# Optimization experiments

Hardware: AMD Instinct MI355X
Metric: run time of the kernel (lower is better)

## Reference

```python
import jax, jax.numpy as jnp
import numpy as np

NUM_HEADS = 4
SPATIAL_DS = 2
EPS = 1e-5


def setup_inputs() -> dict:
    key = jax.random.key(0)
    ks = jax.random.split(key, 6)
    B, C, H, W = 8, 256, 64, 64
    hd = C // NUM_HEADS
    return {
        "x": jax.random.normal(ks[0], (B, C, H, W), jnp.float32),
        "gn_w": jnp.ones((C,), jnp.float32),
        "gn_b": jnp.zeros((C,), jnp.float32),
        "wq": jax.random.normal(ks[1], (C, C), jnp.float32) * (C ** -0.5),
        "wk": jax.random.normal(ks[2], (hd, C), jnp.float32) * (C ** -0.5),
        "wv": jax.random.normal(ks[3], (hd, C), jnp.float32) * (C ** -0.5),
        "wo": jax.random.normal(ks[4], (C, C), jnp.float32) * (C ** -0.5),
        "gamma": jnp.full((C,), 1e-4, jnp.float32),
    }


def reference(x, gn_w, gn_b, wq, wk, wv, wo, gamma):
    B, C, H, W = x.shape
    hd = C // NUM_HEADS
    scale = hd ** -0.5
    ds = SPATIAL_DS

    # GroupNorm with 1 group: normalize over (C,H,W) per sample, per-channel affine
    mu = jnp.mean(x, axis=(1, 2, 3), keepdims=True)
    var = jnp.var(x, axis=(1, 2, 3), keepdims=True)
    xn = (x - mu) * jax.lax.rsqrt(var + EPS)
    xn = xn * gn_w[None, :, None, None] + gn_b[None, :, None, None]

    # Q projection (1x1 conv == channel matmul): (B, heads, N, hd)
    q = jnp.einsum('oc,bchw->bohw', wq, xn).reshape(B, NUM_HEADS, hd, H * W)
    q = jnp.swapaxes(q, 2, 3)  # (B, h, N, hd)

    # AvgPool2d(ds, ds) on normalized input for K/V
    Hd, Wd = H // ds, W // ds
    x_ds = xn.reshape(B, C, Hd, ds, Wd, ds).mean(axis=(3, 5))

    k = jnp.einsum('oc,bchw->bohw', wk, x_ds).reshape(B, hd, Hd * Wd)
    k = jnp.swapaxes(k, 1, 2)  # (B, M, hd) single shared head
    v = jnp.einsum('oc,bchw->bohw', wv, x_ds).reshape(B, hd, Hd * Wd)
    v = jnp.swapaxes(v, 1, 2)  # (B, M, hd)

    # Multi-query attention: queries per-head, shared K/V
    attn = jnp.einsum('bhnd,bmd->bhnm', q, k) * scale
    attn = jax.nn.softmax(attn, axis=-1)
    out = jnp.einsum('bhnm,bmd->bhnd', attn, v)  # (B, h, N, hd)

    out = jnp.swapaxes(out, 2, 3).reshape(B, C, H, W)
    out = jnp.einsum('oc,bchw->bohw', wo, out)

    return x + out * gamma[None, :, None, None]
```

## Files before the change

kernel.cpp:

```cpp
#include <hip/hip_runtime.h>


#define CNT_INV (1.0f/1048576.0f)
#define EPSV 1e-5f
#define QSCALE 0.18033688f

#define WS_STATS 0
#define WS_XNT   64
#define WS_XDS   4194368
#define WS_K     5242944
#define WS_V     5505088
#define WS_WQB   5767232
#define WS_WKV   5800000
#define WS_WOB   5816384

typedef __attribute__((ext_vector_type(8))) short bf8_t;
typedef __attribute__((ext_vector_type(4))) float f4_t;

static __device__ __forceinline__ unsigned fbits(float f) {
  union { float f; unsigned u; } v; v.f = f; return v.u;
}
static __device__ __forceinline__ unsigned short f2bf(float f) {
  unsigned u = fbits(f);
  return (unsigned short)((u + 0x7fffu + ((u >> 16) & 1u)) >> 16);
}
static __device__ __forceinline__ unsigned pk_rnd(float a, float b) {
  return __builtin_amdgcn_perm(fbits(b) + 0x8000u, fbits(a) + 0x8000u, 0x07060302u);
}
static __device__ __forceinline__ unsigned pk_tr(float a, float b) {
  return __builtin_amdgcn_perm(fbits(b), fbits(a), 0x07060302u);
}
static __device__ __forceinline__ float bf2f(unsigned short h) {
  union { unsigned u; float f; } v; v.u = ((unsigned)h) << 16; return v.f;
}
static __device__ __forceinline__ float fexp2(float x) {
  float r; asm("v_exp_f32 %0, %1" : "=v"(r) : "v"(x)); return r;
}

__global__ __launch_bounds__(256) void k_prep_stats(const float* __restrict__ x,
                                                    const float* __restrict__ wq,
                                                    const float* __restrict__ wk,
                                                    const float* __restrict__ wv,
                                                    const float* __restrict__ wo,
                                                    float* __restrict__ stats,
                                                    unsigned short* __restrict__ wqb,
                                                    unsigned short* __restrict__ wkvb,
                                                    unsigned short* __restrict__ wob) {
  const int blk = blockIdx.x;
  const int t = threadIdx.x;
  if (blk < 512) {
    const int b = blk >> 6;
    const int chunk = blk & 63;
    const float4* xb = (const float4*)(x + (size_t)b * 1048576 + (size_t)chunk * 16384);
    float s = 0.f, s2 = 0.f;
#pragma unroll
    for (int it = 0; it < 16; ++it) {
      float4 v = xb[it * 256 + t];
      s  += v.x + v.y + v.z + v.w;
      s2 += v.x * v.x + v.y * v.y + v.z * v.z + v.w * v.w;
    }
#pragma unroll
    for (int o = 32; o > 0; o >>= 1) {
      s  += __shfl_down(s, o);
      s2 += __shfl_down(s2, o);
    }
    __shared__ float red[8];
    const int wid = t >> 6;
    if ((t & 63) == 0) { red[wid] = s; red[4 + wid] = s2; }
    __syncthreads();
    if (t == 0) {
      atomicAdd(&stats[b * 2 + 0], red[0] + red[1] + red[2] + red[3]);
      atomicAdd(&stats[b * 2 + 1], red[4] + red[5] + red[6] + red[7]);
    }
  } else {
    const int idx = (blk - 512) * 256 + t;
    if (idx < 65536) wqb[idx] = f2bf(wq[idx]);
    else if (idx < 81920) wkvb[idx - 65536] = f2bf(wk[idx - 65536]);
    else if (idx < 98304) wkvb[idx - 65536] = f2bf(wv[idx - 81920]);
    else if (idx < 163840) wob[idx - 98304] = f2bf(wo[idx - 98304]);
  }
}

__global__ __launch_bounds__(256) void k_xnt(const float* __restrict__ x,
                                             const float* __restrict__ gnw,
                                             const float* __restrict__ gnb,
                                             const float* __restrict__ stats,
                                             unsigned short* __restrict__ xnT,
                                             unsigned short* __restrict__ xdsT) {
  __shared__ unsigned short T[128][72];
  const int t = threadIdx.x;
  const int b = blockIdx.z, c0 = blockIdx.y * 64, hp = blockIdx.x;
  const int n0 = hp * 128;
  const float mu = stats[b * 2 + 0] * CNT_INV;
  const float rstd = rsqrtf(stats[b * 2 + 1] * CNT_INV - mu * mu + EPSV);
  const int n4 = (t & 31) * 4, cl = t >> 5;
  const int wswz = t & 7;
#pragma unroll
  for (int p = 0; p < 8; ++p) {
    const int c = c0 + p * 8 + cl;
    const float gw = gnw[c] * rstd;
    const float gb = gnb[c] - mu * rstd * gnw[c];
    const int pc = (p ^ wswz) * 8 + cl;
    float4 v = *(const float4*)&x[(size_t)(b * 256 + c) * 4096 + n0 + n4];
    T[n4 + 0][pc] = f2bf(v.x * gw + gb);
    T[n4 + 1][pc] = f2bf(v.y * gw + gb);
    T[n4 + 2][pc] = f2bf(v.z * gw + gb);
    T[n4 + 3][pc] = f2bf(v.w * gw + gb);
  }
  __syncthreads();
  {
    const int r = t >> 1, cb4 = (t & 1) * 4;
    const int rswz = (t >> 3) & 7;
    unsigned short* dst = xnT + ((size_t)b * 4096 + n0 + r) * 256 + c0 + cb4 * 8;
#pragma unroll
    for (int u = 0; u < 4; ++u)
      *(uint4*)(dst + u * 8) = *(const uint4*)&T[r][((cb4 + u) ^ rswz) * 8];
  }
  {
    const int wd = t >> 3, c8 = t & 7;
    const int pswz = (wd >> 1) & 7;
    const int pc = (c8 ^ pswz) * 8;
    uint4 u0 = *(const uint4*)&T[2 * wd][pc];
    uint4 u1 = *(const uint4*)&T[2 * wd + 1][pc];
    uint4 u2 = *(const uint4*)&T[64 + 2 * wd][pc];
    uint4 u3 = *(const uint4*)&T[64 + 2 * wd + 1][pc];
    const unsigned* p0 = (const unsigned*)&u0; const unsigned* p1 = (const unsigned*)&u1;
    const unsigned* p2 = (const unsigned*)&u2; const unsigned* p3 = (const unsigned*)&u3;
    unsigned outp[4];
#pragma unroll
    for (int i = 0; i < 4; ++i) {
      float lo = (bf2f((unsigned short)p0[i]) + bf2f((unsigned short)p1[i]) +
                  bf2f((unsigned short)p2[i]) + bf2f((unsigned short)p3[i])) * 0.25f;
      float hi = (bf2f((unsigned short)(p0[i] >> 16)) + bf2f((unsigned short)(p1[i] >> 16)) +
                  bf2f((unsigned short)(p2[i] >> 16)) + bf2f((unsigned short)(p3[i] >> 16))) * 0.25f;
      outp[i] = pk_rnd(lo, hi);
    }
    *(uint4*)(xdsT + ((size_t)b * 1024 + hp * 32 + wd) * 256 + c0 + c8 * 8) = *(uint4*)outp;
  }
}

__global__ __launch_bounds__(256) void k_gemm_kv(const unsigned short* __restrict__ wkvb,
                                                 const unsigned short* __restrict__ xdsT,
                                                 unsigned short* __restrict__ kbf,
                                                 unsigned short* __restrict__ vtbf) {
  __shared__ __align__(16) unsigned short kv[2][64][72];
  const int t = threadIdx.x;
  const int w = t >> 6, l = t & 63, lane16 = l & 15, quad = l >> 4;
  const int m0 = blockIdx.x * 64, b = blockIdx.y;
  const unsigned short* Abase = wkvb + (size_t)(w * 32 + lane16) * 256 + quad * 8;
  const unsigned short* Bbase = xdsT + ((size_t)b * 1024 + m0 + lane16) * 256 + quad * 8;
  f4_t acc[2][4];
#pragma unroll
  for (int i = 0; i < 2; ++i)
#pragma unroll
    for (int j = 0; j < 4; ++j) acc[i][j] = (f4_t){0.f, 0.f, 0.f, 0.f};
  bf8_t Ac[2], Bc[4];
#pragma unroll
  for (int og = 0; og < 2; ++og) Ac[og] = *(const bf8_t*)(Abase + (size_t)og * 16 * 256);
#pragma unroll
  for (int mg = 0; mg < 4; ++mg) Bc[mg] = *(const bf8_t*)(Bbase + (size_t)mg * 16 * 256);
  for (int kc = 0; kc < 256; kc += 32) {
    const int kn = (kc + 32) & 255;
    bf8_t An[2], Bn[4];
#pragma unroll
    for (int og = 0; og < 2; ++og) An[og] = *(const bf8_t*)(Abase + (size_t)og * 16 * 256 + kn);
#pragma unroll
    for (int mg = 0; mg < 4; ++mg) Bn[mg] = *(const bf8_t*)(Bbase + (size_t)mg * 16 * 256 + kn);
#pragma unroll
    for (int og = 0; og < 2; ++og)
#pragma unroll
      for (int mg = 0; mg < 4; ++mg)
        acc[og][mg] = __builtin_amdgcn_mfma_f32_16x16x32_bf16(Ac[og], Bc[mg], acc[og][mg], 0, 0, 0);
#pragma unroll
    for (int og = 0; og < 2; ++og) Ac[og] = An[og];
#pragma unroll
    for (int mg = 0; mg < 4; ++mg) Bc[mg] = Bn[mg];
  }
  if (w < 2) {
#pragma unroll
    for (int og = 0; og < 2; ++og)
#pragma unroll
      for (int mg = 0; mg < 4; ++mg) {
        uint2 p;
        p.x = pk_rnd(acc[og][mg][0], acc[og][mg][1]);
        p.y = pk_rnd(acc[og][mg][2], acc[og][mg][3]);
        *(uint2*)&kv[0][mg * 16 + lane16][w * 32 + og * 16 + quad * 4] = p;
      }
  } else {
#pragma unroll
    for (int og = 0; og < 2; ++og)
#pragma unroll
      for (int mg = 0; mg < 4; ++mg) {
        const int d0 = (w - 2) * 32 + og * 16 + quad * 4;
#pragma unroll
        for (int r = 0; r < 4; ++r)
          kv[1][d0 + r][mg * 16 + lane16] = f2bf(acc[og][mg][r]);
      }
  }
  __syncthreads();
  {
    const int row = t >> 2, q2 = t & 3;
    const int e = row & 7;
    uint4 k0 = *(const uint4*)&kv[0][row][q2 * 16];
    uint4 k1 = *(const uint4*)&kv[0][row][q2 * 16 + 8];
    unsigned short* kd = kbf + (size_t)b * 65536 + (size_t)(m0 + row) * 64;
    *(uint4*)(kd + ((q2 * 2) ^ e) * 8)     = k0;
    *(uint4*)(kd + ((q2 * 2 + 1) ^ e) * 8) = k1;
    uint4 v0 = *(const uint4*)&kv[1][row][q2 * 16];
    uint4 v1 = *(const uint4*)&kv[1][row][q2 * 16 + 8];
    unsigned short* vd = vtbf + (size_t)b * 65536 + (size_t)(blockIdx.x * 2 + (q2 >> 1)) * 2048 +
                         (size_t)row * 32 + (q2 & 1) * 16;
    *(uint4*)vd = v0; *(uint4*)(vd + 8) = v1;
  }
}

__global__ __launch_bounds__(256) void k_fused(const unsigned short* __restrict__ wqb,
                                               const unsigned short* __restrict__ xnT,
                                               const unsigned short* __restrict__ kbf,
                                               const unsigned short* __restrict__ vtbf,
                                               const unsigned short* __restrict__ wob,
                                               const float* __restrict__ x,
                                               const float* __restrict__ gamma,
                                               float* __restrict__ outp) {
  __shared__ __align__(16) unsigned short smem[20480];
  __shared__ __align__(16) unsigned short kst[2][2048];
  __shared__ __align__(16) unsigned short vst[2][2048];
  const int t = threadIdx.x;
  const int w = t >> 6, l = t & 63, lane16 = l & 15, quad = l >> 4;
  const int n0 = blockIdx.x * 64, b = blockIdx.y;
  const int h = w;
  unsigned short* qst = smem + w * 4608;
  unsigned short (*plds)[64][40] = (unsigned short (*)[64][40])(smem + w * 5120);
  unsigned short (*aos)[264] = (unsigned short (*)[264])smem;

  const int sw = w & 1;
  const unsigned short* sbase = (w < 2) ? (kbf + (size_t)b * 65536) : (vtbf + (size_t)b * 65536);
  unsigned short* sdst0 = ((w < 2) ? &kst[0][0] : &vst[0][0]) + sw * 1024 + l * 8;
  unsigned short* sdst1 = ((w < 2) ? &kst[1][0] : &vst[1][0]) + sw * 1024 + l * 8;

#define STAGE_ISSUE(WIN, R0, R1)                                              \
  { const unsigned short* sp = sbase + (size_t)(WIN) * 2048 + sw * 1024 + l * 8; \
    R0 = *(const uint4*)sp; R1 = *(const uint4*)(sp + 512); }
#define STAGE_WRITE(DP, R0, R1)                                               \
  { *(uint4*)(DP) = R0; *(uint4*)((DP) + 512) = R1; }

#define READ_K(BUF, KREG)                                                     \
  {                                                                           \
    _Pragma("unroll")                                                         \
    for (int s = 0; s < 2; ++s) {                                             \
      _Pragma("unroll")                                                       \
      for (int dc = 0; dc < 2; ++dc)                                          \
        KREG[s][dc] = *(const bf8_t*)&kst[BUF][(s * 16 + lane16) * 64 +       \
                                              (((dc * 4 + quad) ^ (lane16 & 7)) * 8)]; \
    }                                                                         \
  }
#define READ_V(BUF, VREG)                                                     \
  {                                                                           \
    _Pragma("unroll")                                                         \
    for (int dg = 0; dg < 4; ++dg)                                            \
      VREG[dg] = *(const bf8_t*)&vst[BUF][(dg * 16 + lane16) * 32 + quad * 8]; \
  }

  const unsigned short* kb = kbf;

  {
    const unsigned short* Abase = wqb + (size_t)(h * 64 + lane16) * 256 + quad * 8;
    const unsigned short* Bbase = xnT + ((size_t)b * 4096 + n0 + lane16) * 256 + quad * 8;
    f4_t qacc[4][4];
#pragma unroll
    for (int i = 0; i < 4; ++i)
#pragma unroll
      for (int j = 0; j < 4; ++j) qacc[i][j] = (f4_t){0.f, 0.f, 0.f, 0.f};
    for (int kc = 0; kc < 256; kc += 32) {
      bf8_t A[4], Bf[4];
#pragma unroll
      for (int og = 0; og < 4; ++og) A[og] = *(const bf8_t*)(Abase + (size_t)og * 16 * 256 + kc);
#pragma unroll
      for (int ng = 0; ng < 4; ++ng) Bf[ng] = *(const bf8_t*)(Bbase + (size_t)ng * 16 * 256 + kc);
#pragma unroll
      for (int og = 0; og < 4; ++og)
#pragma unroll
        for (int ng = 0; ng < 4; ++ng)
          qacc[og][ng] = __builtin_amdgcn_mfma_f32_16x16x32_bf16(A[og], Bf[ng], qacc[og][ng], 0, 0, 0);
    }
#pragma unroll
    for (int og = 0; og < 4; ++og)
#pragma unroll
      for (int ng = 0; ng < 4; ++ng) {
        uint2 p;
        p.x = pk_rnd(qacc[og][ng][0] * QSCALE, qacc[og][ng][1] * QSCALE);
        p.y = pk_rnd(qacc[og][ng][2] * QSCALE, qacc[og][ng][3] * QSCALE);
        *(uint2*)&qst[(ng * 16 + lane16) * 72 + og * 16 + quad * 4] = p;
      }
  }
  bf8_t Qf[4][2];
#pragma unroll
  for (int qg = 0; qg < 4; ++qg)
#pragma unroll
    for (int dc = 0; dc < 2; ++dc)
      Qf[qg][dc] = *(const bf8_t*)&qst[(qg * 16 + lane16) * 72 + dc * 32 + quad * 8];
  __syncthreads();

  f4_t O[4][4];
#pragma unroll
  for (int dg = 0; dg < 4; ++dg)
#pragma unroll
    for (int qg = 0; qg < 4; ++qg) O[dg][qg] = (f4_t){0.f, 0.f, 0.f, 0.f};
  f4_t O4[4];
#pragma unroll
  for (int qg = 0; qg < 4; ++qg) O4[qg] = (f4_t){0.f, 0.f, 0.f, 0.f};
  const short onebf = (lane16 == 0) ? (short)0x3F80 : (short)0;
  const bf8_t Aone = {onebf, onebf, onebf, onebf, onebf, onebf, onebf, onebf};

#define SSTEP(KREG, BUF)                                                      \
  {                                                                           \
    _Pragma("unroll")                                                         \
    for (int qg = 0; qg < 4; ++qg) {                                          \
      _Pragma("unroll")                                                       \
      for (int s = 0; s < 2; ++s) {                                           \
        f4_t S = (f4_t){0.f, 0.f, 0.f, 0.f};                                  \
        S = __builtin_amdgcn_mfma_f32_16x16x32_bf16(KREG[s][0], Qf[qg][0], S, 0, 0, 0); \
        S = __builtin_amdgcn_mfma_f32_16x16x32_bf16(KREG[s][1], Qf[qg][1], S, 0, 0, 0); \
        float e0 = fexp2(S[0]);                                               \
        float e1 = fexp2(S[1]);                                               \
        float e2 = fexp2(S[2]);                                               \
        float e3 = fexp2(S[3]);                                               \
        uint2 p; p.x = pk_tr(e0, e1); p.y = pk_tr(e2, e3);                    \
        *(uint2*)&plds[BUF][qg * 16 + lane16][s * 16 + quad * 4] = p;         \
      }                                                                       \
    }                                                                         \
  }

  {
    uint4 a0, a1, b0, b1;
    STAGE_ISSUE(0, a0, a1);
    STAGE_ISSUE(1, b0, b1);
    STAGE_WRITE(sdst0, a0, a1);
    STAGE_WRITE(sdst1, b0, b1);
  }
  __syncthreads();

  bf8_t Kc[2][2], Vc[4];
  READ_K(0, Kc);
  SSTEP(Kc, 0);
  READ_V(0, Vc);
  __syncthreads();

  for (int it = 1; it < 32; ++it) {
    const int cur = it & 1, pb = cur ^ 1;
    uint4 g0, g1;
    if (it < 31) STAGE_ISSUE(it + 1, g0, g1);
    bf8_t Pf[4];
#pragma unroll
    for (int qg = 0; qg < 4; ++qg)
      Pf[qg] = *(const bf8_t*)&plds[pb][qg * 16 + lane16][quad * 8];
    READ_K(cur, Kc);
    bf8_t Vn[4];
    READ_V(cur, Vn);
    __builtin_amdgcn_s_setprio(1);
#pragma unroll
    for (int dg = 0; dg < 4; ++dg)
#pragma unroll
      for (int qg = 0; qg < 4; ++qg)
        O[dg][qg] = __builtin_amdgcn_mfma_f32_16x16x32_bf16(Vc[dg], Pf[qg], O[dg][qg], 0, 0, 0);
#pragma unroll
    for (int qg = 0; qg < 4; ++qg)
      O4[qg] = __builtin_amdgcn_mfma_f32_16x16x32_bf16(Aone, Pf[qg], O4[qg], 0, 0, 0);
    __builtin_amdgcn_s_setprio(0);
    SSTEP(Kc, cur);
#pragma unroll
    for (int dg = 0; dg < 4; ++dg) Vc[dg] = Vn[dg];
    if (it < 31) STAGE_WRITE((cur ? sdst0 : sdst1), g0, g1);
    __syncthreads();
  }
  {
    bf8_t Pf[4];
#pragma unroll
    for (int qg = 0; qg < 4; ++qg)
      Pf[qg] = *(const bf8_t*)&plds[1][qg * 16 + lane16][quad * 8];
    __builtin_amdgcn_s_setprio(1);
#pragma unroll
    for (int dg = 0; dg < 4; ++dg)
#pragma unroll
      for (int qg = 0; qg < 4; ++qg)
        O[dg][qg] = __builtin_amdgcn_mfma_f32_16x16x32_bf16(Vc[dg], Pf[qg], O[dg][qg], 0, 0, 0);
#pragma unroll
    for (int qg = 0; qg < 4; ++qg)
      O4[qg] = __builtin_amdgcn_mfma_f32_16x16x32_bf16(Aone, Pf[qg], O4[qg], 0, 0, 0);
    __builtin_amdgcn_s_setprio(0);
  }
#undef SSTEP
#undef STAGE_ISSUE
#undef STAGE_WRITE
#undef READ_K
#undef READ_V
  (void)kb;

  float rden[4];
#pragma unroll
  for (int qg = 0; qg < 4; ++qg) {
    float d = __shfl(O4[qg][0], lane16);
    rden[qg] = 1.f / d;
  }

  __syncthreads();
#pragma unroll
  for (int dg = 0; dg < 4; ++dg)
#pragma unroll
    for (int qg = 0; qg < 4; ++qg) {
      const int c0 = h * 64 + dg * 16 + quad * 4;
      uint2 p;
      p.x = pk_rnd(O[dg][qg][0] * rden[qg], O[dg][qg][1] * rden[qg]);
      p.y = pk_rnd(O[dg][qg][2] * rden[qg], O[dg][qg][3] * rden[qg]);
      *(uint2*)&aos[qg * 16 + lane16][c0] = p;
    }
  __syncthreads();

  {
    const unsigned short* Wbase = wob + (size_t)(w * 64 + lane16) * 256 + quad * 8;
    f4_t acc[4][4];
#pragma unroll
    for (int i = 0; i < 4; ++i)
#pragma unroll
      for (int j = 0; j < 4; ++j) acc[i][j] = (f4_t){0.f, 0.f, 0.f, 0.f};
    for (int kc = 0; kc < 256; kc += 32) {
      bf8_t A[4], Bf[4];
#pragma unroll
      for (int og = 0; og < 4; ++og) A[og] = *(const bf8_t*)(Wbase + (size_t)og * 16 * 256 + kc);
#pragma unroll
      for (int ng = 0; ng < 4; ++ng) Bf[ng] = *(const bf8_t*)&aos[ng * 16 + lane16][kc + quad * 8];
#pragma unroll
      for (int og = 0; og < 4; ++og)
#pragma unroll
        for (int ng = 0; ng < 4; ++ng)
          acc[og][ng] = __builtin_amdgcn_mfma_f32_16x16x32_bf16(A[og], Bf[ng], acc[og][ng], 0, 0, 0);
    }
#pragma unroll
    for (int og = 0; og < 4; ++og) {
      float4 g4 = *(const float4*)&gamma[w * 64 + og * 16 + quad * 4];
      const float g[4] = {g4.x, g4.y, g4.z, g4.w};
#pragma unroll
      for (int ng = 0; ng < 4; ++ng) {
        const int n = n0 + ng * 16 + lane16;
#pragma unroll
        for (int r = 0; r < 4; ++r) {
          const int o = w * 64 + og * 16 + quad * 4 + r;
          const size_t ix = ((size_t)(b * 256 + o)) * 4096 + n;
          outp[ix] = x[ix] + g[r] * acc[og][ng][r];
        }
      }
    }
  }
}

extern "C" void kernel_launch(void* const* d_in, const int* in_sizes, int n_in,
                              void* d_out, int out_size, void* d_ws, size_t ws_size,
                              hipStream_t stream) {
  const float* x     = (const float*)d_in[0];
  const float* gnw   = (const float*)d_in[1];
  const float* gnb   = (const float*)d_in[2];
  const float* wq    = (const float*)d_in[3];
  const float* wk    = (const float*)d_in[4];
  const float* wv    = (const float*)d_in[5];
  const float* wo    = (const float*)d_in[6];
  const float* gamma = (const float*)d_in[7];
  float* out = (float*)d_out;
  float* ws  = (float*)d_ws;
  unsigned short* xnT  = (unsigned short*)(ws + WS_XNT);
  unsigned short* xdsT = (unsigned short*)(ws + WS_XDS);
  unsigned short* kbf  = (unsigned short*)(ws + WS_K);
  unsigned short* vtbf = (unsigned short*)(ws + WS_V);
  unsigned short* wqb  = (unsigned short*)(ws + WS_WQB);
  unsigned short* wkvb = (unsigned short*)(ws + WS_WKV);
  unsigned short* wob  = (unsigned short*)(ws + WS_WOB);

  hipMemsetAsync(ws, 0, 256, stream);
  k_prep_stats<<<1152, 256, 0, stream>>>(x, wq, wk, wv, wo, ws + WS_STATS, wqb, wkvb, wob);
  k_xnt<<<dim3(32, 4, 8), 256, 0, stream>>>(x, gnw, gnb, ws + WS_STATS, xnT, xdsT);
  k_gemm_kv<<<dim3(16, 8), 256, 0, stream>>>(wkvb, xdsT, kbf, vtbf);
  k_fused<<<dim3(64, 8), 256, 0, stream>>>(wqb, xnT, kbf, vtbf, wob, x, gamma, out);
}
```

Before: 194.1 us.

## Fold groupnorm affine and avgpool into consumer GEMMs, merge transpose into prep kernel

The raw x is now transposed to bf16 in the stats/prep kernel, which removes the separate normalize-and-transpose kernel and the pooled buffer. The GroupNorm affine is applied on the fly to the B operands in the Q GEMM inside the fused kernel. The 2x2 average pool plus affine is computed while loading operands in the KV GEMM, which now uses smaller tiles across more blocks. This saves a launch and a global round trip, at the cost of extra ALU work in the GEMM inner loops, more uncoalesced 4-way loads for the pooling, and bf16 rounding applied before normalization rather than after.

```diff
diff --git a/kernel.cpp b/kernel.cpp
--- a/kernel.cpp
+++ b/kernel.cpp
@@ -7,7 +7,6 @@
 
 #define WS_STATS 0
 #define WS_XNT   64
-#define WS_XDS   4194368
 #define WS_K     5242944
 #define WS_V     5505088
 #define WS_WQB   5767232
@@ -37,15 +36,47 @@
   float r; asm("v_exp_f32 %0, %1" : "=v"(r) : "v"(x)); return r;
 }
 
-__global__ __launch_bounds__(256) void k_prep_stats(const float* __restrict__ x,
-                                                    const float* __restrict__ wq,
-                                                    const float* __restrict__ wk,
-                                                    const float* __restrict__ wv,
-                                                    const float* __restrict__ wo,
-                                                    float* __restrict__ stats,
-                                                    unsigned short* __restrict__ wqb,
-                                                    unsigned short* __restrict__ wkvb,
-                                                    unsigned short* __restrict__ wob) {
+static __device__ __forceinline__ bf8_t affine8(bf8_t r, const float* a8, const float* b8) {
+  union { bf8_t v; unsigned short u[8]; unsigned w[4]; } in, out;
+  in.v = r;
+#pragma unroll
+  for (int i = 0; i < 4; ++i) {
+    float lo = fmaf(bf2f(in.u[2 * i]),     a8[2 * i],     b8[2 * i]);
+    float hi = fmaf(bf2f(in.u[2 * i + 1]), a8[2 * i + 1], b8[2 * i + 1]);
+    out.w[i] = pk_rnd(lo, hi);
+  }
+  return out.v;
+}
+
+static __device__ __forceinline__ bf8_t pool_affine(bf8_t s00, bf8_t s01, bf8_t s10, bf8_t s11,
+                                                    const float* a4, const float* b8) {
+  union { bf8_t v; unsigned short u[8]; unsigned w[4]; } x00, x01, x10, x11, out;
+  x00.v = s00; x01.v = s01; x10.v = s10; x11.v = s11;
+#pragma unroll
+  for (int i = 0; i < 4; ++i) {
+    float lo = (bf2f(x00.u[2 * i]) + bf2f(x01.u[2 * i])) +
+               (bf2f(x10.u[2 * i]) + bf2f(x11.u[2 * i]));
+    float hi = (bf2f(x00.u[2 * i + 1]) + bf2f(x01.u[2 * i + 1])) +
+               (bf2f(x10.u[2 * i + 1]) + bf2f(x11.u[2 * i + 1]));
+    lo = fmaf(lo, a4[2 * i],     b8[2 * i]);
+    hi = fmaf(hi, a4[2 * i + 1], b8[2 * i + 1]);
+    out.w[i] = pk_rnd(lo, hi);
+  }
+  return out.v;
+}
+
+__global__ __launch_bounds__(256) void k_prep(const float* __restrict__ x,
+                                              const float* __restrict__ wq,
+                                              const float* __restrict__ wk,
+                                              const float* __restrict__ wv,
+                                              const float* __restrict__ wo,
+                                              float* __restrict__ stats,
+                                              unsigned short* __restrict__ wqb,
+                                              unsigned short* __restrict__ wkvb,
+                                              unsigned short* __restrict__ wob,
+                                              unsigned short* __restrict__ xtb) {
+  __shared__ unsigned short T[128][72];
+  __shared__ float red[8];
   const int blk = blockIdx.x;
   const int t = threadIdx.x;
   if (blk < 512) {
@@ -64,7 +95,6 @@
       s  += __shfl_down(s, o);
       s2 += __shfl_down(s2, o);
     }
-    __shared__ float red[8];
     const int wid = t >> 6;
     if ((t & 63) == 0) { red[wid] = s; red[4 + wid] = s2; }
     __syncthreads();
@@ -72,150 +102,144 @@
       atomicAdd(&stats[b * 2 + 0], red[0] + red[1] + red[2] + red[3]);
       atomicAdd(&stats[b * 2 + 1], red[4] + red[5] + red[6] + red[7]);
     }
-  } else {
+  } else if (blk < 1152) {
     const int idx = (blk - 512) * 256 + t;
     if (idx < 65536) wqb[idx] = f2bf(wq[idx]);
     else if (idx < 81920) wkvb[idx - 65536] = f2bf(wk[idx - 65536]);
     else if (idx < 98304) wkvb[idx - 65536] = f2bf(wv[idx - 81920]);
     else if (idx < 163840) wob[idx - 98304] = f2bf(wo[idx - 98304]);
-  }
-}
-
-__global__ __launch_bounds__(256) void k_xnt(const float* __restrict__ x,
-                                             const float* __restrict__ gnw,
-                                             const float* __restrict__ gnb,
-                                             const float* __restrict__ stats,
-                                             unsigned short* __restrict__ xnT,
-                                             unsigned short* __restrict__ xdsT) {
-  __shared__ unsigned short T[128][72];
+  } else {
+    const int idx = blk - 1152;
+    const int hp = idx & 31, cq = (idx >> 5) & 3, b = idx >> 7;
+    const int c0 = cq * 64, n0 = hp * 128;
+    const int n4 = (t & 31) * 4, cl = t >> 5;
+    const int wswz = t & 7;
+#pragma unroll
+    for (int p = 0; p < 8; ++p) {
+      const int c = c0 + p * 8 + cl;
+      const int pc = (p ^ wswz) * 8 + cl;
+      float4 v = *(const float4*)&x[(size_t)(b * 256 + c) * 4096 + n0 + n4];
+      T[n4 + 0][pc] = f2bf(v.x);
+      T[n4 + 1][pc] = f2bf(v.y);
+      T[n4 + 2][pc] = f2bf(v.z);
+      T[n4 + 3][pc] = f2bf(v.w);
+    }
+    __syncthreads();
+    {
+      const int r = t >> 1, cb4 = (t & 1) * 4;
+      const int rswz = (t >> 3) & 7;
+      unsigned short* dst = xtb + ((size_t)b * 4096 + n0 + r) * 256 + c0 + cb4 * 8;
+#pragma unroll
+      for (int u = 0; u < 4; ++u)
+        *(uint4*)(dst + u * 8) = *(const uint4*)&T[r][((cb4 + u) ^ rswz) * 8];
+    }
+  }
+}
+
+__global__ __launch_bounds__(256) void k_gemm_kv(const unsigned short* __restrict__ wkvb,
+                                                 const unsigned short* __restrict__ xtb,
+                                                 const float* __restrict__ gnw,
+                                                 const float* __restrict__ gnb,
+                                                 const float* __restrict__ stats,
+                                                 unsigned short* __restrict__ kbf,
+                                                 unsigned short* __restrict__ vtbf) {
+  __shared__ __align__(16) unsigned short kv0[32][72];
+  __shared__ __align__(16) unsigned short kv1[64][40];
   const int t = threadIdx.x;
-  const int b = blockIdx.z, c0 = blockIdx.y * 64, hp = blockIdx.x;
-  const int n0 = hp * 128;
+  const int w = t >> 6, l = t & 63, lane16 = l & 15, quad = l >> 4;
+  const int m0 = blockIdx.x * 32, b = blockIdx.y;
+  const int kvsel = w >> 1, wh = w & 1;
   const float mu = stats[b * 2 + 0] * CNT_INV;
   const float rstd = rsqrtf(stats[b * 2 + 1] * CNT_INV - mu * mu + EPSV);
-  const int n4 = (t & 31) * 4, cl = t >> 5;
-  const int wswz = t & 7;
-#pragma unroll
-  for (int p = 0; p < 8; ++p) {
-    const int c = c0 + p * 8 + cl;
-    const float gw = gnw[c] * rstd;
-    const float gb = gnb[c] - mu * rstd * gnw[c];
-    const int pc = (p ^ wswz) * 8 + cl;
-    float4 v = *(const float4*)&x[(size_t)(b * 256 + c) * 4096 + n0 + n4];
-    T[n4 + 0][pc] = f2bf(v.x * gw + gb);
-    T[n4 + 1][pc] = f2bf(v.y * gw + gb);
-    T[n4 + 2][pc] = f2bf(v.z * gw + gb);
-    T[n4 + 3][pc] = f2bf(v.w * gw + gb);
-  }
-  __syncthreads();
-  {
-    const int r = t >> 1, cb4 = (t & 1) * 4;
-    const int rswz = (t >> 3) & 7;
-    unsigned short* dst = xnT + ((size_t)b * 4096 + n0 + r) * 256 + c0 + cb4 * 8;
-#pragma unroll
-    for (int u = 0; u < 4; ++u)
-      *(uint4*)(dst + u * 8) = *(const uint4*)&T[r][((cb4 + u) ^ rswz) * 8];
-  }
-  {
-    const int wd = t >> 3, c8 = t & 7;
-    const int pswz = (wd >> 1) & 7;
-    const int pc = (c8 ^ pswz) * 8;
-    uint4 u0 = *(const uint4*)&T[2 * wd][pc];
-    uint4 u1 = *(const uint4*)&T[2 * wd + 1][pc];
-    uint4 u2 = *(const uint4*)&T[64 + 2 * wd][pc];
-    uint4 u3 = *(const uint4*)&T[64 + 2 * wd + 1][pc];
-    const unsigned* p0 = (const unsigned*)&u0; const unsigned* p1 = (const unsigned*)&u1;
-    const unsigned* p2 = (const unsigned*)&u2; const unsigned* p3 = (const unsigned*)&u3;
-    unsigned outp[4];
-#pragma unroll
-    for (int i = 0; i < 4; ++i) {
-      float lo = (bf2f((unsigned short)p0[i]) + bf2f((unsigned short)p1[i]) +
-                  bf2f((unsigned short)p2[i]) + bf2f((unsigned short)p3[i])) * 0.25f;
-      float hi = (bf2f((unsigned short)(p0[i] >> 16)) + bf2f((unsigned short)(p1[i] >> 16)) +
-                  bf2f((unsigned short)(p2[i] >> 16)) + bf2f((unsigned short)(p3[i] >> 16))) * 0.25f;
-      outp[i] = pk_rnd(lo, hi);
-    }
-    *(uint4*)(xdsT + ((size_t)b * 1024 + hp * 32 + wd) * 256 + c0 + c8 * 8) = *(uint4*)outp;
-  }
-}
-
-__global__ __launch_bounds__(256) void k_gemm_kv(const unsigned short* __restrict__ wkvb,
-                                                 const unsigned short* __restrict__ xdsT,
-                                                 unsigned short* __restrict__ kbf,
-                                                 unsigned short* __restrict__ vtbf) {
-  __shared__ __align__(16) unsigned short kv[2][64][72];
-  const int t = threadIdx.x;
-  const int w = t >> 6, l = t & 63, lane16 = l & 15, quad = l >> 4;
-  const int m0 = blockIdx.x * 64, b = blockIdx.y;
-  const unsigned short* Abase = wkvb + (size_t)(w * 32 + lane16) * 256 + quad * 8;
-  const unsigned short* Bbase = xdsT + ((size_t)b * 1024 + m0 + lane16) * 256 + quad * 8;
-  f4_t acc[2][4];
+
+  const unsigned short* Abase = wkvb + (size_t)kvsel * 16384 +
+                                (size_t)(wh * 32 + lane16) * 256 + quad * 8;
+  const unsigned short* B00[2];
+#pragma unroll
+  for (int mg = 0; mg < 2; ++mg) {
+    const int m = m0 + mg * 16 + lane16;
+    const int nb = (m >> 5) * 128 + (m & 31) * 2;
+    B00[mg] = xtb + ((size_t)b * 4096 + nb) * 256 + quad * 8;
+  }
+
+  f4_t acc[2][2];
 #pragma unroll
   for (int i = 0; i < 2; ++i)
 #pragma unroll
-    for (int j = 0; j < 4; ++j) acc[i][j] = (f4_t){0.f, 0.f, 0.f, 0.f};
-  bf8_t Ac[2], Bc[4];
-#pragma unroll
-  for (int og = 0; og < 2; ++og) Ac[og] = *(const bf8_t*)(Abase + (size_t)og * 16 * 256);
-#pragma unroll
-  for (int mg = 0; mg < 4; ++mg) Bc[mg] = *(const bf8_t*)(Bbase + (size_t)mg * 16 * 256);
+    for (int j = 0; j < 2; ++j) acc[i][j] = (f4_t){0.f, 0.f, 0.f, 0.f};
+
   for (int kc = 0; kc < 256; kc += 32) {
-    const int kn = (kc + 32) & 255;
-    bf8_t An[2], Bn[4];
-#pragma unroll
-    for (int og = 0; og < 2; ++og) An[og] = *(const bf8_t*)(Abase + (size_t)og * 16 * 256 + kn);
-#pragma unroll
-    for (int mg = 0; mg < 4; ++mg) Bn[mg] = *(const bf8_t*)(Bbase + (size_t)mg * 16 * 256 + kn);
+    const int cb = kc + quad * 8;
+    float4 g0 = *(const float4*)&gnw[cb];
+    float4 g1 = *(const float4*)&gnw[cb + 4];
+    float4 h0 = *(const float4*)&gnb[cb];
+    float4 h1 = *(const float4*)&gnb[cb + 4];
+    float a4[8], b8[8];
+    const float gg[8] = {g0.x, g0.y, g0.z, g0.w, g1.x, g1.y, g1.z, g1.w};
+    const float hh[8] = {h0.x, h0.y, h0.z, h0.w, h1.x, h1.y, h1.z, h1.w};
+#pragma unroll
+    for (int j = 0; j < 8; ++j) {
+      const float a = gg[j] * rstd;
+      a4[j] = a * 0.25f;
+      b8[j] = hh[j] - mu * a;
+    }
+    bf8_t Bf[2];
+#pragma unroll
+    for (int mg = 0; mg < 2; ++mg) {
+      const unsigned short* p = B00[mg] + kc;
+      bf8_t s00 = *(const bf8_t*)p;
+      bf8_t s01 = *(const bf8_t*)(p + 256);
+      bf8_t s10 = *(const bf8_t*)(p + 64 * 256);
+      bf8_t s11 = *(const bf8_t*)(p + 65 * 256);
+      Bf[mg] = pool_affine(s00, s01, s10, s11, a4, b8);
+    }
+    bf8_t A[2];
+#pragma unroll
+    for (int og = 0; og < 2; ++og) A[og] = *(const bf8_t*)(Abase + (size_t)og * 16 * 256 + kc);
 #pragma unroll
     for (int og = 0; og < 2; ++og)
 #pragma unroll
-      for (int mg = 0; mg < 4; ++mg)
-        acc[og][mg] = __builtin_amdgcn_mfma_f32_16x16x32_bf16(Ac[og], Bc[mg], acc[og][mg], 0, 0, 0);
-#pragma unroll
-    for (int og = 0; og < 2; ++og) Ac[og] = An[og];
-#pragma unroll
-    for (int mg = 0; mg < 4; ++mg) Bc[mg] = Bn[mg];
-  }
+      for (int mg = 0; mg < 2; ++mg)
+        acc[og][mg] = __builtin_amdgcn_mfma_f32_16x16x32_bf16(A[og], Bf[mg], acc[og][mg], 0, 0, 0);
+  }
+
   if (w < 2) {
 #pragma unroll
     for (int og = 0; og < 2; ++og)
 #pragma unroll
-      for (int mg = 0; mg < 4; ++mg) {
+      for (int mg = 0; mg < 2; ++mg) {
         uint2 p;
         p.x = pk_rnd(acc[og][mg][0], acc[og][mg][1]);
         p.y = pk_rnd(acc[og][mg][2], acc[og][mg][3]);
-        *(uint2*)&kv[0][mg * 16 + lane16][w * 32 + og * 16 + quad * 4] = p;
+        *(uint2*)&kv0[mg * 16 + lane16][wh * 32 + og * 16 + quad * 4] = p;
       }
   } else {
 #pragma unroll
     for (int og = 0; og < 2; ++og)
 #pragma unroll
-      for (int mg = 0; mg < 4; ++mg) {
-        const int d0 = (w - 2) * 32 + og * 16 + quad * 4;
+      for (int mg = 0; mg < 2; ++mg) {
+        const int d0 = wh * 32 + og * 16 + quad * 4;
 #pragma unroll
         for (int r = 0; r < 4; ++r)
-          kv[1][d0 + r][mg * 16 + lane16] = f2bf(acc[og][mg][r]);
+          kv1[d0 + r][mg * 16 + lane16] = f2bf(acc[og][mg][r]);
       }
   }
   __syncthreads();
   {
-    const int row = t >> 2, q2 = t & 3;
-    const int e = row & 7;
-    uint4 k0 = *(const uint4*)&kv[0][row][q2 * 16];
-    uint4 k1 = *(const uint4*)&kv[0][row][q2 * 16 + 8];
-    unsigned short* kd = kbf + (size_t)b * 65536 + (size_t)(m0 + row) * 64;
-    *(uint4*)(kd + ((q2 * 2) ^ e) * 8)     = k0;
-    *(uint4*)(kd + ((q2 * 2 + 1) ^ e) * 8) = k1;
-    uint4 v0 = *(const uint4*)&kv[1][row][q2 * 16];
-    uint4 v1 = *(const uint4*)&kv[1][row][q2 * 16 + 8];
-    unsigned short* vd = vtbf + (size_t)b * 65536 + (size_t)(blockIdx.x * 2 + (q2 >> 1)) * 2048 +
-                         (size_t)row * 32 + (q2 & 1) * 16;
-    *(uint4*)vd = v0; *(uint4*)(vd + 8) = v1;
+    const int rowk = t >> 3, ch = t & 7, e = rowk & 7;
+    *(uint4*)(kbf + (size_t)b * 65536 + (size_t)(m0 + rowk) * 64 + ((ch ^ e) * 8)) =
+        *(const uint4*)&kv0[rowk][ch * 8];
+    const int rowd = t >> 2, q = t & 3;
+    *(uint4*)(vtbf + (size_t)b * 65536 + (size_t)(m0 >> 5) * 2048 + (size_t)rowd * 32 + q * 8) =
+        *(const uint4*)&kv1[rowd][q * 8];
   }
 }
 
 __global__ __launch_bounds__(256) void k_fused(const unsigned short* __restrict__ wqb,
-                                               const unsigned short* __restrict__ xnT,
+                                               const unsigned short* __restrict__ xtb,
+                                               const float* __restrict__ gnw,
+                                               const float* __restrict__ gnb,
+                                               const float* __restrict__ stats,
                                                const unsigned short* __restrict__ kbf,
                                                const unsigned short* __restrict__ vtbf,
                                                const unsigned short* __restrict__ wob,
@@ -233,6 +257,9 @@
   unsigned short (*plds)[64][40] = (unsigned short (*)[64][40])(smem + w * 5120);
   unsigned short (*aos)[264] = (unsigned short (*)[264])smem;
 
+  const float mu = stats[b * 2 + 0] * CNT_INV;
+  const float rstd = rsqrtf(stats[b * 2 + 1] * CNT_INV - mu * mu + EPSV);
+
   const int sw = w & 1;
   const unsigned short* sbase = (w < 2) ? (kbf + (size_t)b * 65536) : (vtbf + (size_t)b * 65536);
   unsigned short* sdst0 = ((w < 2) ? &kst[0][0] : &vst[0][0]) + sw * 1024 + l * 8;
@@ -261,22 +288,36 @@
       VREG[dg] = *(const bf8_t*)&vst[BUF][(dg * 16 + lane16) * 32 + quad * 8]; \
   }
 
-  const unsigned short* kb = kbf;
-
   {
     const unsigned short* Abase = wqb + (size_t)(h * 64 + lane16) * 256 + quad * 8;
-    const unsigned short* Bbase = xnT + ((size_t)b * 4096 + n0 + lane16) * 256 + quad * 8;
+    const unsigned short* Bbase = xtb + ((size_t)b * 4096 + n0 + lane16) * 256 + quad * 8;
     f4_t qacc[4][4];
 #pragma unroll
     for (int i = 0; i < 4; ++i)
 #pragma unroll
       for (int j = 0; j < 4; ++j) qacc[i][j] = (f4_t){0.f, 0.f, 0.f, 0.f};
     for (int kc = 0; kc < 256; kc += 32) {
+      const int cb = kc + quad * 8;
+      float4 g0 = *(const float4*)&gnw[cb];
+      float4 g1 = *(const float4*)&gnw[cb + 4];
+      float4 h0 = *(const float4*)&gnb[cb];
+      float4 h1 = *(const float4*)&gnb[cb + 4];
+      float a8[8], b8[8];
+      const float gg[8] = {g0.x, g0.y, g0.z, g0.w, g1.x, g1.y, g1.z, g1.w};
+      const float hh[8] = {h0.x, h0.y, h0.z, h0.w, h1.x, h1.y, h1.z, h1.w};
+#pragma unroll
+      for (int j = 0; j < 8; ++j) {
+        a8[j] = gg[j] * rstd;
+        b8[j] = hh[j] - mu * a8[j];
+      }
       bf8_t A[4], Bf[4];
 #pragma unroll
       for (int og = 0; og < 4; ++og) A[og] = *(const bf8_t*)(Abase + (size_t)og * 16 * 256 + kc);
 #pragma unroll
-      for (int ng = 0; ng < 4; ++ng) Bf[ng] = *(const bf8_t*)(Bbase + (size_t)ng * 16 * 256 + kc);
+      for (int ng = 0; ng < 4; ++ng) {
+        bf8_t raw = *(const bf8_t*)(Bbase + (size_t)ng * 16 * 256 + kc);
+        Bf[ng] = affine8(raw, a8, b8);
+      }
 #pragma unroll
       for (int og = 0; og < 4; ++og)
 #pragma unroll
@@ -394,7 +435,6 @@
 #undef STAGE_WRITE
 #undef READ_K
 #undef READ_V
-  (void)kb;
 
   float rden[4];
 #pragma unroll
@@ -466,8 +506,7 @@
   const float* gamma = (const float*)d_in[7];
   float* out = (float*)d_out;
   float* ws  = (float*)d_ws;
-  unsigned short* xnT  = (unsigned short*)(ws + WS_XNT);
-  unsigned short* xdsT = (unsigned short*)(ws + WS_XDS);
+  unsigned short* xtb  = (unsigned short*)(ws + WS_XNT);
   unsigned short* kbf  = (unsigned short*)(ws + WS_K);
   unsigned short* vtbf = (unsigned short*)(ws + WS_V);
   unsigned short* wqb  = (unsigned short*)(ws + WS_WQB);
@@ -475,8 +514,7 @@
   unsigned short* wob  = (unsigned short*)(ws + WS_WOB);
 
   hipMemsetAsync(ws, 0, 256, stream);
-  k_prep_stats<<<1152, 256, 0, stream>>>(x, wq, wk, wv, wo, ws + WS_STATS, wqb, wkvb, wob);
-  k_xnt<<<dim3(32, 4, 8), 256, 0, stream>>>(x, gnw, gnb, ws + WS_STATS, xnT, xdsT);
-  k_gemm_kv<<<dim3(16, 8), 256, 0, stream>>>(wkvb, xdsT, kbf, vtbf);
-  k_fused<<<dim3(64, 8), 256, 0, stream>>>(wqb, xnT, kbf, vtbf, wob, x, gamma, out);
-}
+  k_prep<<<2176, 256, 0, stream>>>(x, wq, wk, wv, wo, ws + WS_STATS, wqb, wkvb, wob, xtb);
+  k_gemm_kv<<<dim3(32, 8), 256, 0, stream>>>(wkvb, xtb, gnw, gnb, ws + WS_STATS, kbf, vtbf);
+  k_fused<<<dim3(64, 8), 256, 0, stream>>>(wqb, xtb, gnw, gnb, ws + WS_STATS, kbf, vtbf, wob, x, gamma, out);
+}
```

Result: slower. 201.3 us (+3.7%).
